# Performance work log

Hardware: AMD Instinct MI355X
Metric: run time of the kernel (lower is better)

The kernel has to match this reference:

```python
import jax, jax.numpy as jnp
import numpy as np

EPS = 1e-5

def layer_norm(x, g, b):
    m = jnp.mean(x, axis=-1, keepdims=True)
    v = jnp.var(x, axis=-1, keepdims=True)
    return (x - m) * jax.lax.rsqrt(v + EPS) * g + b

def setup_inputs() -> dict:
    key = jax.random.key(0)
    ks = jax.random.split(key, 10)
    A, T, c_s, c_z, c_atom, c_pair = 1024, 256, 384, 128, 128, 16
    tok = jax.random.randint(ks[0], (A,), 0, T)
    a2t = jax.nn.one_hot(tok, T, dtype=jnp.float32)  # [A, T] one-hot atom->token map
    return {
        "atom_to_token_index": a2t,
        "cl": jax.random.normal(ks[1], (A, c_atom), jnp.float32),
        "plm": jax.random.normal(ks[2], (A, A, c_pair), jnp.float32),
        "ql": jax.random.normal(ks[3], (A, c_atom), jnp.float32),
        "s_trunk": jax.random.normal(ks[4], (T, c_s), jnp.float32),
        "zij": jax.random.normal(ks[5], (T, T, c_z), jnp.float32),
        "rl": jax.random.normal(ks[6], (A, 3), jnp.float32),
        "ln_s_g": jnp.ones((c_s,), jnp.float32),
        "ln_s_b": jnp.zeros((c_s,), jnp.float32),
        "W_s": jax.random.normal(ks[7], (c_s, c_atom), jnp.float32) / np.sqrt(c_s),
        "ln_z_g": jnp.ones((c_z,), jnp.float32),
        "ln_z_b": jnp.zeros((c_z,), jnp.float32),
        "W_z": jax.random.normal(ks[8], (c_z, c_pair), jnp.float32) / np.sqrt(c_z),
        "W_r": jax.random.normal(ks[9], (3, c_atom), jnp.float32) / np.sqrt(3.0),
    }

def reference(atom_to_token_index, cl, plm, ql, s_trunk, zij, rl,
              ln_s_g, ln_s_b, W_s, ln_z_g, ln_z_b, W_z, W_r):
    a2t = atom_to_token_index  # [A, T]
    # token -> atom gather of single rep: sum_t a2t[a,t] * s_trunk[t,:]  -> [A, c_s]
    s_atom = jnp.einsum('at,tc->ac', a2t, s_trunk)
    cl = cl + layer_norm(s_atom, ln_s_g, ln_s_b) @ W_s  # [A, c_atom]
    # token-pair -> atom-pair gather: sum_{t,u} a2t[a,t] a2t[b,u] zij[t,u,:]
    # factored into two one-hot contractions (same math as the dense one-hot outer product)
    z_half = jnp.einsum('at,tuz->auz', a2t, zij)      # [A, T, c_z]
    z_atom = jnp.einsum('auz,bu->abz', z_half, a2t)    # [A, A, c_z]
    plm = plm + layer_norm(z_atom, ln_z_g, ln_z_b) @ W_z  # [A, A, c_pair]
    ql = ql + rl @ W_r  # [A, c_atom]
    return (cl, plm, ql)
```

## Files before the change

### kernel.cpp

```cpp
#include <hip/hip_runtime.h>

#define A_N 1024
#define T_N 256
#define CS 384
#define CZ 128
#define CA 128
#define CP 16
#define LN_EPS 1e-5f

#define ZROWS 64
#define ZPAD 132

__global__ void tok_kernel(const float* __restrict__ a2t, int* __restrict__ tok) {
    int a = blockIdx.x;
    int t = threadIdx.x;
    if (a2t[a * T_N + t] > 0.5f) tok[a] = t;
}

__global__ void prep_gwbw_kernel(const float* __restrict__ g,
                                 const float* __restrict__ b,
                                 const float* __restrict__ W_z,
                                 float* __restrict__ Gw,
                                 float* __restrict__ Bw) {
    __shared__ float pg[16][16], pb[16][16];
    int t = threadIdx.x;
    int j = t & 15, seg = t >> 4;
    float sg = 0.f, sb = 0.f;
    #pragma unroll
    for (int i = 0; i < 8; ++i) {
        int k = seg * 8 + i;
        float w = W_z[k * CP + j];
        sg = fmaf(g[k], w, sg);
        sb = fmaf(b[k], w, sb);
    }
    pg[seg][j] = sg; pb[seg][j] = sb;
    __syncthreads();
    if (t < 16) {
        float a = 0.f, c = 0.f;
        #pragma unroll
        for (int s = 0; s < 16; ++s) { a += pg[s][t]; c += pb[s][t]; }
        Gw[t] = a; Bw[t] = c;
    }
}

__global__ void s_phase_kernel(const float* __restrict__ s_trunk,
                               const float* __restrict__ g,
                               const float* __restrict__ b,
                               const float* __restrict__ W_s,
                               float* __restrict__ Ys) {
    int t = blockIdx.x;
    int tid = threadIdx.x;
    __shared__ float xs[CS];
    __shared__ float rs[128], rq[128];
    float sum = 0.f, sq = 0.f;
    for (int j = 0; j < 3; ++j) {
        float v = s_trunk[t * CS + j * 128 + tid];
        xs[j * 128 + tid] = v;
        sum += v; sq += v * v;
    }
    rs[tid] = sum; rq[tid] = sq;
    __syncthreads();
    for (int s = 64; s > 0; s >>= 1) {
        if (tid < s) { rs[tid] += rs[tid + s]; rq[tid] += rq[tid + s]; }
        __syncthreads();
    }
    float m = rs[0] * (1.f / CS);
    float var = rq[0] * (1.f / CS) - m * m;
    float rstd = rsqrtf(var + LN_EPS);
    float acc = 0.f;
    for (int k = 0; k < CS; ++k) {
        float zn = (xs[k] - m) * rstd * g[k] + b[k];
        acc = fmaf(zn, W_s[k * CA + tid], acc);
    }
    Ys[t * CA + tid] = acc;
}

__global__ __launch_bounds__(256) void z_phase2_kernel(
        const float* __restrict__ zij,
        const float* __restrict__ g,
        const float* __restrict__ W_z,
        const float* __restrict__ Gw,
        const float* __restrict__ Bw,
        float* __restrict__ Yz) {
    __shared__ float xs[ZROWS * ZPAD];
    __shared__ float wgt[CP * ZPAD];
    __shared__ float2 parts[ZROWS][4];
    __shared__ float msh[ZROWS], rsh[ZROWS];

    int t = threadIdx.x;
    size_t base = (size_t)blockIdx.x * ZROWS * CZ;

    const float4* zv = (const float4*)(zij + base);
    #pragma unroll
    for (int n = 0; n < 8; ++n) {
        int idx = n * 256 + t;
        int r = idx >> 5, c = idx & 31;
        float4 v = zv[idx];
        *(float4*)&xs[r * ZPAD + c * 4] = v;
    }
    #pragma unroll
    for (int n = 0; n < 8; ++n) {
        int idx = n * 256 + t;
        int k = idx >> 4, j = idx & 15;
        wgt[j * ZPAD + k] = g[k] * W_z[idx];
    }
    __syncthreads();

    {
        int r = t >> 2, q = t & 3;
        const float* row = &xs[r * ZPAD + q * 32];
        float s = 0.f, ss = 0.f;
        #pragma unroll
        for (int i = 0; i < 8; ++i) {
            float4 v = *(const float4*)&row[i * 4];
            s += v.x + v.y + v.z + v.w;
            ss += v.x * v.x + v.y * v.y + v.z * v.z + v.w * v.w;
        }
        parts[r][q] = make_float2(s, ss);
    }
    __syncthreads();
    if (t < ZROWS) {
        float s = 0.f, ss = 0.f;
        #pragma unroll
        for (int q = 0; q < 4; ++q) { float2 p = parts[t][q]; s += p.x; ss += p.y; }
        float m = s * (1.f / CZ);
        float var = ss * (1.f / CZ) - m * m;
        msh[t] = m;
        rsh[t] = rsqrtf(var + LN_EPS);
    }
    __syncthreads();

    int j = t & 15, rg = t >> 4;
    float acc[4] = {0.f, 0.f, 0.f, 0.f};
    const float* wrow = &wgt[j * ZPAD];
    #pragma unroll 4
    for (int k4 = 0; k4 < 32; ++k4) {
        float4 w = *(const float4*)&wrow[k4 * 4];
        #pragma unroll
        for (int rr = 0; rr < 4; ++rr) {
            float4 x = *(const float4*)&xs[(rg * 4 + rr) * ZPAD + k4 * 4];
            acc[rr] = fmaf(x.x, w.x, acc[rr]);
            acc[rr] = fmaf(x.y, w.y, acc[rr]);
            acc[rr] = fmaf(x.z, w.z, acc[rr]);
            acc[rr] = fmaf(x.w, w.w, acc[rr]);
        }
    }
    float gwj = Gw[j], bwj = Bw[j];
    #pragma unroll
    for (int rr = 0; rr < 4; ++rr) {
        int r = rg * 4 + rr;
        float y = rsh[r] * (acc[rr] - msh[r] * gwj) + bwj;
        size_t grow = (size_t)blockIdx.x * ZROWS + r;
        Yz[grow * CP + j] = y;
    }
}

__global__ void cl_final_kernel(const float* __restrict__ cl,
                                const float* __restrict__ Ys,
                                const int* __restrict__ tok,
                                float* __restrict__ out) {
    int i = blockIdx.x * blockDim.x + threadIdx.x;
    int a = i >> 7;
    int c = i & 127;
    out[i] = cl[i] + Ys[tok[a] * CA + c];
}

__global__ void plm_final_kernel(const float* __restrict__ plm,
                                 const float* __restrict__ Yz,
                                 const int* __restrict__ tok,
                                 float* __restrict__ out) {
    int i = blockIdx.x * blockDim.x + threadIdx.x;
    int p  = i >> 2;
    int c4 = i & 3;
    int a = p >> 10;
    int b = p & 1023;
    int ta = tok[a];
    int tb = tok[b];
    float4 pv = ((const float4*)plm)[i];
    float4 yv = ((const float4*)(Yz + (size_t)(ta * T_N + tb) * CP))[c4];
    float4 o;
    o.x = pv.x + yv.x; o.y = pv.y + yv.y;
    o.z = pv.z + yv.z; o.w = pv.w + yv.w;
    ((float4*)out)[i] = o;
}

__global__ void ql_final_kernel(const float* __restrict__ ql,
                                const float* __restrict__ rl,
                                const float* __restrict__ W_r,
                                float* __restrict__ out) {
    int i = blockIdx.x * blockDim.x + threadIdx.x;
    int a = i >> 7;
    int c = i & 127;
    float r0 = rl[a * 3 + 0], r1 = rl[a * 3 + 1], r2 = rl[a * 3 + 2];
    out[i] = ql[i] + r0 * W_r[c] + r1 * W_r[CA + c] + r2 * W_r[2 * CA + c];
}

extern "C" void kernel_launch(void* const* d_in, const int* in_sizes, int n_in,
                              void* d_out, int out_size, void* d_ws, size_t ws_size,
                              hipStream_t stream) {
    const float* a2t     = (const float*)d_in[0];
    const float* cl      = (const float*)d_in[1];
    const float* plm     = (const float*)d_in[2];
    const float* ql      = (const float*)d_in[3];
    const float* s_trunk = (const float*)d_in[4];
    const float* zij     = (const float*)d_in[5];
    const float* rl      = (const float*)d_in[6];
    const float* ln_s_g  = (const float*)d_in[7];
    const float* ln_s_b  = (const float*)d_in[8];
    const float* W_s     = (const float*)d_in[9];
    const float* ln_z_g  = (const float*)d_in[10];
    const float* ln_z_b  = (const float*)d_in[11];
    const float* W_z     = (const float*)d_in[12];
    const float* W_r     = (const float*)d_in[13];

    int*   tok = (int*)d_ws;
    float* Ys  = (float*)((char*)d_ws + 4096);
    float* Yz  = (float*)((char*)d_ws + 4096 + 131072 * 4);
    float* Gw  = Yz + (size_t)T_N * T_N * CP;
    float* Bw  = Gw + 16;

    float* out_cl  = (float*)d_out;
    float* out_plm = out_cl + A_N * CA;
    float* out_ql  = out_plm + (size_t)A_N * A_N * CP;

    tok_kernel<<<A_N, T_N, 0, stream>>>(a2t, tok);
    prep_gwbw_kernel<<<1, 256, 0, stream>>>(ln_z_g, ln_z_b, W_z, Gw, Bw);
    s_phase_kernel<<<T_N, 128, 0, stream>>>(s_trunk, ln_s_g, ln_s_b, W_s, Ys);
    z_phase2_kernel<<<(T_N * T_N) / ZROWS, 256, 0, stream>>>(zij, ln_z_g, W_z, Gw, Bw, Yz);
    cl_final_kernel<<<(A_N * CA) / 256, 256, 0, stream>>>(cl, Ys, tok, out_cl);
    plm_final_kernel<<<((size_t)A_N * A_N * CP / 4) / 256, 256, 0, stream>>>(plm, Yz, tok, out_plm);
    ql_final_kernel<<<(A_N * CA) / 256, 256, 0, stream>>>(ql, rl, W_r, out_ql);
}
```

Before: 205.9 us.

## Fuse small kernels into atom, z and plm kernels to cut launches

The launch sequence shrinks from seven kernels to three. Token lookup, the s-layernorm projection, and the cl and ql outputs are merged into one per-atom kernel, and the Gw/Bw prep is folded into each z block. The plm kernel now reads the row token once per block instead of decoding it per thread. The aim is to remove launch overhead and intermediate round trips, at the cost of recomputing the s-projection per atom (4x redundant) and the Gw/Bw sums in every z block.

```diff
diff --git a/kernel.cpp b/kernel.cpp
--- a/kernel.cpp
+++ b/kernel.cpp
@@ -11,81 +11,75 @@
 #define ZROWS 64
 #define ZPAD 132
 
-__global__ void tok_kernel(const float* __restrict__ a2t, int* __restrict__ tok) {
-    int a = blockIdx.x;
-    int t = threadIdx.x;
-    if (a2t[a * T_N + t] > 0.5f) tok[a] = t;
-}
-
-__global__ void prep_gwbw_kernel(const float* __restrict__ g,
-                                 const float* __restrict__ b,
-                                 const float* __restrict__ W_z,
-                                 float* __restrict__ Gw,
-                                 float* __restrict__ Bw) {
-    __shared__ float pg[16][16], pb[16][16];
-    int t = threadIdx.x;
-    int j = t & 15, seg = t >> 4;
-    float sg = 0.f, sb = 0.f;
-    #pragma unroll
-    for (int i = 0; i < 8; ++i) {
-        int k = seg * 8 + i;
-        float w = W_z[k * CP + j];
-        sg = fmaf(g[k], w, sg);
-        sb = fmaf(b[k], w, sb);
-    }
-    pg[seg][j] = sg; pb[seg][j] = sb;
-    __syncthreads();
-    if (t < 16) {
-        float a = 0.f, c = 0.f;
-        #pragma unroll
-        for (int s = 0; s < 16; ++s) { a += pg[s][t]; c += pb[s][t]; }
-        Gw[t] = a; Bw[t] = c;
-    }
-}
-
-__global__ void s_phase_kernel(const float* __restrict__ s_trunk,
-                               const float* __restrict__ g,
-                               const float* __restrict__ b,
-                               const float* __restrict__ W_s,
-                               float* __restrict__ Ys) {
-    int t = blockIdx.x;
-    int tid = threadIdx.x;
+__global__ __launch_bounds__(128) void atom_kernel(
+        const float* __restrict__ a2t,
+        const float* __restrict__ cl,
+        const float* __restrict__ ql,
+        const float* __restrict__ s_trunk,
+        const float* __restrict__ rl,
+        const float* __restrict__ g,
+        const float* __restrict__ b,
+        const float* __restrict__ W_s,
+        const float* __restrict__ W_r,
+        int* __restrict__ tok,
+        float* __restrict__ out_cl,
+        float* __restrict__ out_ql) {
+    int a = blockIdx.x, tid = threadIdx.x;
+    __shared__ int ta_sh;
     __shared__ float xs[CS];
-    __shared__ float rs[128], rq[128];
+    __shared__ float2 wred[2];
+
+    float v0 = a2t[a * T_N + tid];
+    float v1 = a2t[a * T_N + 128 + tid];
+    if (v0 > 0.5f) ta_sh = tid;
+    if (v1 > 0.5f) ta_sh = 128 + tid;
+    __syncthreads();
+    int ta = ta_sh;
+    if (tid == 0) tok[a] = ta;
+
     float sum = 0.f, sq = 0.f;
+    #pragma unroll
     for (int j = 0; j < 3; ++j) {
-        float v = s_trunk[t * CS + j * 128 + tid];
+        float v = s_trunk[ta * CS + j * 128 + tid];
         xs[j * 128 + tid] = v;
         sum += v; sq += v * v;
     }
-    rs[tid] = sum; rq[tid] = sq;
-    __syncthreads();
-    for (int s = 64; s > 0; s >>= 1) {
-        if (tid < s) { rs[tid] += rs[tid + s]; rq[tid] += rq[tid + s]; }
-        __syncthreads();
-    }
-    float m = rs[0] * (1.f / CS);
-    float var = rq[0] * (1.f / CS) - m * m;
-    float rstd = rsqrtf(var + LN_EPS);
+    #pragma unroll
+    for (int off = 32; off > 0; off >>= 1) {
+        sum += __shfl_down(sum, off);
+        sq  += __shfl_down(sq,  off);
+    }
+    if ((tid & 63) == 0) wred[tid >> 6] = make_float2(sum, sq);
+    __syncthreads();
+    float s  = wred[0].x + wred[1].x;
+    float ss = wred[0].y + wred[1].y;
+    float m = s * (1.f / CS);
+    float rstd = rsqrtf(ss * (1.f / CS) - m * m + LN_EPS);
+
     float acc = 0.f;
     for (int k = 0; k < CS; ++k) {
         float zn = (xs[k] - m) * rstd * g[k] + b[k];
         acc = fmaf(zn, W_s[k * CA + tid], acc);
     }
-    Ys[t * CA + tid] = acc;
-}
-
-__global__ __launch_bounds__(256) void z_phase2_kernel(
+    out_cl[a * CA + tid] = cl[a * CA + tid] + acc;
+
+    float r0 = rl[a * 3 + 0], r1 = rl[a * 3 + 1], r2 = rl[a * 3 + 2];
+    out_ql[a * CA + tid] = ql[a * CA + tid]
+                         + r0 * W_r[tid] + r1 * W_r[CA + tid] + r2 * W_r[2 * CA + tid];
+}
+
+__global__ __launch_bounds__(256) void z_kernel(
         const float* __restrict__ zij,
         const float* __restrict__ g,
+        const float* __restrict__ b,
         const float* __restrict__ W_z,
-        const float* __restrict__ Gw,
-        const float* __restrict__ Bw,
         float* __restrict__ Yz) {
     __shared__ float xs[ZROWS * ZPAD];
     __shared__ float wgt[CP * ZPAD];
     __shared__ float2 parts[ZROWS][4];
     __shared__ float msh[ZROWS], rsh[ZROWS];
+    __shared__ float2 gb_part[16][16];
+    __shared__ float Gw_sh[CP], Bw_sh[CP];
 
     int t = threadIdx.x;
     size_t base = (size_t)blockIdx.x * ZROWS * CZ;
@@ -95,17 +89,29 @@
     for (int n = 0; n < 8; ++n) {
         int idx = n * 256 + t;
         int r = idx >> 5, c = idx & 31;
-        float4 v = zv[idx];
-        *(float4*)&xs[r * ZPAD + c * 4] = v;
-    }
-    #pragma unroll
-    for (int n = 0; n < 8; ++n) {
-        int idx = n * 256 + t;
-        int k = idx >> 4, j = idx & 15;
-        wgt[j * ZPAD + k] = g[k] * W_z[idx];
-    }
-    __syncthreads();
-
+        *(float4*)&xs[r * ZPAD + c * 4] = zv[idx];
+    }
+    {
+        int j = t & 15, seg = t >> 4;
+        float sg = 0.f, sb = 0.f;
+        #pragma unroll
+        for (int i = 0; i < 8; ++i) {
+            int k = seg * 8 + i;
+            float w = W_z[k * CP + j];
+            float gw = g[k] * w;
+            wgt[j * ZPAD + k] = gw;
+            sg += gw;
+            sb = fmaf(b[k], w, sb);
+        }
+        gb_part[seg][j] = make_float2(sg, sb);
+    }
+    __syncthreads();
+    if (t < CP) {
+        float sg = 0.f, sb = 0.f;
+        #pragma unroll
+        for (int s = 0; s < 16; ++s) { float2 p = gb_part[s][t]; sg += p.x; sb += p.y; }
+        Gw_sh[t] = sg; Bw_sh[t] = sb;
+    }
     {
         int r = t >> 2, q = t & 3;
         const float* row = &xs[r * ZPAD + q * 32];
@@ -124,9 +130,8 @@
         #pragma unroll
         for (int q = 0; q < 4; ++q) { float2 p = parts[t][q]; s += p.x; ss += p.y; }
         float m = s * (1.f / CZ);
-        float var = ss * (1.f / CZ) - m * m;
         msh[t] = m;
-        rsh[t] = rsqrtf(var + LN_EPS);
+        rsh[t] = rsqrtf(ss * (1.f / CZ) - m * m + LN_EPS);
     }
     __syncthreads();
 
@@ -145,7 +150,7 @@
             acc[rr] = fmaf(x.w, w.w, acc[rr]);
         }
     }
-    float gwj = Gw[j], bwj = Bw[j];
+    float gwj = Gw_sh[j], bwj = Bw_sh[j];
     #pragma unroll
     for (int rr = 0; rr < 4; ++rr) {
         int r = rg * 4 + rr;
@@ -155,44 +160,22 @@
     }
 }
 
-__global__ void cl_final_kernel(const float* __restrict__ cl,
-                                const float* __restrict__ Ys,
-                                const int* __restrict__ tok,
-                                float* __restrict__ out) {
-    int i = blockIdx.x * blockDim.x + threadIdx.x;
-    int a = i >> 7;
-    int c = i & 127;
-    out[i] = cl[i] + Ys[tok[a] * CA + c];
-}
-
-__global__ void plm_final_kernel(const float* __restrict__ plm,
-                                 const float* __restrict__ Yz,
-                                 const int* __restrict__ tok,
-                                 float* __restrict__ out) {
-    int i = blockIdx.x * blockDim.x + threadIdx.x;
-    int p  = i >> 2;
-    int c4 = i & 3;
-    int a = p >> 10;
-    int b = p & 1023;
-    int ta = tok[a];
-    int tb = tok[b];
+__global__ __launch_bounds__(256) void plm_kernel(
+        const float* __restrict__ plm,
+        const float* __restrict__ Yz,
+        const int* __restrict__ tok,
+        float* __restrict__ out) {
+    int tid = threadIdx.x;
+    size_t i = (size_t)blockIdx.x * 256 + tid;
+    int ta = tok[blockIdx.x >> 4];
+    int bb = ((blockIdx.x & 15) << 6) + (tid >> 2);
+    int tb = tok[bb];
     float4 pv = ((const float4*)plm)[i];
-    float4 yv = ((const float4*)(Yz + (size_t)(ta * T_N + tb) * CP))[c4];
+    float4 yv = ((const float4*)(Yz + (size_t)(ta * T_N + tb) * CP))[tid & 3];
     float4 o;
     o.x = pv.x + yv.x; o.y = pv.y + yv.y;
     o.z = pv.z + yv.z; o.w = pv.w + yv.w;
     ((float4*)out)[i] = o;
-}
-
-__global__ void ql_final_kernel(const float* __restrict__ ql,
-                                const float* __restrict__ rl,
-                                const float* __restrict__ W_r,
-                                float* __restrict__ out) {
-    int i = blockIdx.x * blockDim.x + threadIdx.x;
-    int a = i >> 7;
-    int c = i & 127;
-    float r0 = rl[a * 3 + 0], r1 = rl[a * 3 + 1], r2 = rl[a * 3 + 2];
-    out[i] = ql[i] + r0 * W_r[c] + r1 * W_r[CA + c] + r2 * W_r[2 * CA + c];
 }
 
 extern "C" void kernel_launch(void* const* d_in, const int* in_sizes, int n_in,
@@ -214,20 +197,15 @@
     const float* W_r     = (const float*)d_in[13];
 
     int*   tok = (int*)d_ws;
-    float* Ys  = (float*)((char*)d_ws + 4096);
-    float* Yz  = (float*)((char*)d_ws + 4096 + 131072 * 4);
-    float* Gw  = Yz + (size_t)T_N * T_N * CP;
-    float* Bw  = Gw + 16;
+    float* Yz  = (float*)((char*)d_ws + 4096);
 
     float* out_cl  = (float*)d_out;
     float* out_plm = out_cl + A_N * CA;
     float* out_ql  = out_plm + (size_t)A_N * A_N * CP;
 
-    tok_kernel<<<A_N, T_N, 0, stream>>>(a2t, tok);
-    prep_gwbw_kernel<<<1, 256, 0, stream>>>(ln_z_g, ln_z_b, W_z, Gw, Bw);
-    s_phase_kernel<<<T_N, 128, 0, stream>>>(s_trunk, ln_s_g, ln_s_b, W_s, Ys);
-    z_phase2_kernel<<<(T_N * T_N) / ZROWS, 256, 0, stream>>>(zij, ln_z_g, W_z, Gw, Bw, Yz);
-    cl_final_kernel<<<(A_N * CA) / 256, 256, 0, stream>>>(cl, Ys, tok, out_cl);
-    plm_final_kernel<<<((size_t)A_N * A_N * CP / 4) / 256, 256, 0, stream>>>(plm, Yz, tok, out_plm);
-    ql_final_kernel<<<(A_N * CA) / 256, 256, 0, stream>>>(ql, rl, W_r, out_ql);
-}
+    atom_kernel<<<A_N, 128, 0, stream>>>(a2t, cl, ql, s_trunk, rl,
+                                         ln_s_g, ln_s_b, W_s, W_r,
+                                         tok, out_cl, out_ql);
+    z_kernel<<<(T_N * T_N) / ZROWS, 256, 0, stream>>>(zij, ln_z_g, ln_z_b, W_z, Yz);
+    plm_kernel<<<((size_t)A_N * A_N * CP / 4) / 256, 256, 0, stream>>>(plm, Yz, tok, out_plm);
+}
```

Result: faster. 200.9 us (-2.4%).
